# Performance work log

Measured on AMD Instinct MI355X. Metric: run time of the kernel, lower is better.

The kernel has to match this reference:

```python
import jax, jax.numpy as jnp
import numpy as np

DIM = 64
N_ITER = 2
NUM_USR = 50000
NUM_ENT = 200000
NUM_REL = 32
N_NEIGHBOR = 16
BATCH = 4096


def setup_inputs() -> dict:
    key = jax.random.key(0)
    ks = jax.random.split(key, 12)
    u = jax.random.randint(ks[0], (BATCH,), 0, NUM_USR)
    v = jax.random.randint(ks[1], (BATCH,), 0, NUM_ENT)
    adj = jax.random.randint(ks[2], (NUM_ENT, N_NEIGHBOR), 0, NUM_ENT)
    rel_adj = jax.random.randint(ks[3], (NUM_ENT, N_NEIGHBOR), 0, NUM_REL + 1)
    usr_emb = jax.random.normal(ks[4], (NUM_USR, DIM), dtype=jnp.float32)
    ent_emb = jax.random.normal(ks[5], (NUM_ENT, DIM), dtype=jnp.float32)
    rel_emb = jax.random.normal(ks[6], (NUM_REL + 1, DIM), dtype=jnp.float32)
    # per-hop aggregator Linear(dim, dim) weights (applied as x @ W + b)
    scale = 1.0 / np.sqrt(DIM)
    W0 = jax.random.uniform(ks[7], (DIM, DIM), jnp.float32, -scale, scale)
    b0 = jax.random.uniform(ks[8], (DIM,), jnp.float32, -scale, scale)
    W1 = jax.random.uniform(ks[9], (DIM, DIM), jnp.float32, -scale, scale)
    b1 = jax.random.uniform(ks[10], (DIM,), jnp.float32, -scale, scale)
    return {"u": u, "v": v, "adj": adj, "rel_adj": rel_adj,
            "usr_emb": usr_emb, "ent_emb": ent_emb, "rel_emb": rel_emb,
            "W0": W0, "b0": b0, "W1": W1, "b1": b1}


def reference(u, v, adj, rel_adj, usr_emb, ent_emb, rel_emb, W0, b0, W1, b1):
    B = u.shape[0]
    user = usr_emb[u]  # [B, D]

    # multi-hop neighbor index expansion
    entities = [v[:, None]]            # hop h: [B, n^h]
    relations = []
    for h in range(N_ITER):
        ne = adj[entities[h]].reshape(B, -1)      # [B, n^(h+1)]
        nr = rel_adj[entities[h]].reshape(B, -1)
        entities.append(ne)
        relations.append(nr)

    ent_vecs = [ent_emb[e] for e in entities]     # [B, n^h, D]
    rel_vecs = [rel_emb[r] for r in relations]

    Ws, bs = [W0, W1], [b0, b1]
    for i in range(N_ITER):
        act = jnp.tanh if i == N_ITER - 1 else jax.nn.sigmoid
        nxt = []
        for hop in range(N_ITER - i):
            sv = ent_vecs[hop]                                        # [B, m, D]
            nv = ent_vecs[hop + 1].reshape(B, -1, N_NEIGHBOR, DIM)    # [B, m, n, D]
            nr = rel_vecs[hop].reshape(B, -1, N_NEIGHBOR, DIM)        # [B, m, n, D]
            # user-relation attention over neighbors
            scores = jnp.einsum('bd,bmnd->bmn', user, nr)
            attn = jax.nn.softmax(scores, axis=-1)
            agg = jnp.einsum('bmn,bmnd->bmd', attn, nv)
            out = act((sv + agg) @ Ws[i] + bs[i])
            nxt.append(out)
        ent_vecs = nxt

    item = ent_vecs[0].reshape(B, DIM)
    return jax.nn.sigmoid(jnp.sum(user * item, axis=1))
```

## Files before the change

### kernel.cpp

```cpp
#include <hip/hip_runtime.h>

#define DIMN 64
#define NNB 16
#define NREL 33
#define WPB 4
#define XSTR 68

typedef float  floatx4 __attribute__((ext_vector_type(4)));
typedef short  shortx8 __attribute__((ext_vector_type(8)));

__device__ __forceinline__ float bcastf(float x, int lane) {
    return __int_as_float(__builtin_amdgcn_readlane(__float_as_int(x), lane));
}

__global__ void prep_w0_frags(const float* __restrict__ W0, unsigned short* __restrict__ wsp) {
    const int tid = blockIdx.x * blockDim.x + threadIdx.x;
    if (tid >= 512) return;
    const int l = tid & 63;
    const int t = (tid >> 6) & 3;
    const int ks = tid >> 8;
    const int k0 = ks * 32 + (l >> 4) * 8;
    const int n  = t * 16 + (l & 15);
    const unsigned base = ((unsigned)(ks * 4 + t) * 64 + l) * 8;
    #pragma unroll
    for (int j = 0; j < 8; ++j) {
        const float x = W0[(k0 + j) * DIMN + n];
        const unsigned u  = __float_as_uint(x);
        const unsigned uh = u & 0xFFFF0000u;
        const float lf = x - __uint_as_float(uh);
        wsp[base + j]        = (unsigned short)(u >> 16);
        wsp[4096 + base + j] = (unsigned short)(__float_as_uint(lf) >> 16);
    }
}

__global__ __launch_bounds__(64 * WPB, 4)
void kgs_kernel(const int* __restrict__ u, const int* __restrict__ v,
                const int* __restrict__ adj, const int* __restrict__ rel_adj,
                const float* __restrict__ usr_emb, const float* __restrict__ ent_emb,
                const float* __restrict__ rel_emb,
                const float* __restrict__ W0, const float* __restrict__ b0,
                const float* __restrict__ W1, const float* __restrict__ b1,
                const unsigned short* __restrict__ wsp,
                float* __restrict__ out, int B)
{
    const int tid = threadIdx.x;
    const int wid = tid >> 6;
    const int d   = tid & 63;
    int b = blockIdx.x * WPB + wid;
    if (b >= B) b = B - 1;
    const int n16 = d & 15;

    __shared__ __align__(16) float user_sh[WPB][DIMN];
    __shared__ float ur_sh[WPB][NREL + 7];
    __shared__ __align__(16) float xbuf[WPB][NNB * XSTR];

    const int uu = u[b];
    const int vv = v[b];

    const float user_d = usr_emb[uu * DIMN + d];
    const int e1n = adj[vv * NNB + n16];
    const int r1n = rel_adj[vv * NNB + n16];
    user_sh[wid][d] = user_d;

    if (d < NREL) {
        const float* re = rel_emb + d * DIMN;
        float acc = 0.f;
        #pragma unroll
        for (int k = 0; k < DIMN; k += 4) {
            const float4 uk = *(const float4*)(&user_sh[wid][k]);
            const float4 rk = *(const float4*)(re + k);
            acc = fmaf(uk.x, rk.x, acc);
            acc = fmaf(uk.y, rk.y, acc);
            acc = fmaf(uk.z, rk.z, acc);
            acc = fmaf(uk.w, rk.w, acc);
        }
        ur_sh[wid][d] = acc;
    }

    float sv_r[NNB];
    int   e2n_r[NNB], r2n_r[NNB];
    #pragma unroll
    for (int m = 0; m < NNB; ++m) {
        const int em = __builtin_amdgcn_readlane(e1n, m);
        sv_r[m]  = ent_emb[(size_t)em * DIMN + d];
        e2n_r[m] = adj[em * NNB + n16];
        r2n_r[m] = rel_adj[em * NNB + n16];
    }

    float attn[NNB];
    #pragma unroll
    for (int m = 0; m < NNB; ++m) {
        const float e = __expf(ur_sh[wid][r2n_r[m]]);
        float s = e;
        s += __shfl_xor(s, 1);
        s += __shfl_xor(s, 2);
        s += __shfl_xor(s, 4);
        s += __shfl_xor(s, 8);
        attn[m] = e * __builtin_amdgcn_rcpf(s);
    }

    float agg[NNB];
    #pragma unroll
    for (int m = 0; m < NNB; ++m) agg[m] = 0.f;
    #pragma unroll
    for (int m = 0; m < NNB; ++m) {
        #pragma unroll
        for (int n = 0; n < NNB; ++n) {
            const int en = __builtin_amdgcn_readlane(e2n_r[m], n);
            const float* rp = ent_emb + (size_t)en * DIMN;
            agg[m] = fmaf(bcastf(attn[m], n), rp[d], agg[m]);
        }
    }

    #pragma unroll
    for (int m = 0; m < NNB; ++m)
        xbuf[wid][m * XSTR + d] = sv_r[m] + agg[m];

    shortx8 Ahi[2], Alo[2];
    #pragma unroll
    for (int ks = 0; ks < 2; ++ks) {
        const float* ar = &xbuf[wid][(d & 15) * XSTR + ((d >> 4) * 8) + ks * 32];
        const floatx4 xa = *(const floatx4*)ar;
        const floatx4 xb = *(const floatx4*)(ar + 4);
        unsigned uh[8], ul[8];
        #pragma unroll
        for (int j = 0; j < 8; ++j) {
            const float x = (j < 4) ? xa[j] : xb[j - 4];
            const unsigned ub = __float_as_uint(x);
            uh[j] = ub & 0xFFFF0000u;
            ul[j] = __float_as_uint(x - __uint_as_float(uh[j]));
        }
        union { int i[4]; shortx8 s; } ch, cl;
        #pragma unroll
        for (int p = 0; p < 4; ++p) {
            ch.i[p] = (int)(uh[2 * p + 1] | (uh[2 * p] >> 16));
            cl.i[p] = (int)((ul[2 * p + 1] & 0xFFFF0000u) | (ul[2 * p] >> 16));
        }
        Ahi[ks] = ch.s;
        Alo[ks] = cl.s;
    }

    const shortx8* wf = (const shortx8*)wsp;
    floatx4 acc[4];
    #pragma unroll
    for (int t = 0; t < 4; ++t) acc[t] = (floatx4){0.f, 0.f, 0.f, 0.f};
    #pragma unroll
    for (int t = 0; t < 4; ++t) {
        #pragma unroll
        for (int ks = 0; ks < 2; ++ks) {
            const int f = ks * 4 + t;
            const shortx8 bhi = wf[f * 64 + d];
            const shortx8 blo = wf[512 + f * 64 + d];
            acc[t] = __builtin_amdgcn_mfma_f32_16x16x32_bf16(Ahi[ks], bhi, acc[t], 0, 0, 0);
            acc[t] = __builtin_amdgcn_mfma_f32_16x16x32_bf16(Ahi[ks], blo, acc[t], 0, 0, 0);
            acc[t] = __builtin_amdgcn_mfma_f32_16x16x32_bf16(Alo[ks], bhi, acc[t], 0, 0, 0);
        }
    }

    #pragma unroll
    for (int t = 0; t < 4; ++t) {
        const float bv = b0[t * 16 + (d & 15)];
        #pragma unroll
        for (int reg = 0; reg < 4; ++reg) {
            const float o = acc[t][reg] + bv;
            const float h = 1.f / (1.f + __expf(-o));
            const int m = (d >> 4) * 4 + reg;
            xbuf[wid][m * XSTR + t * 16 + (d & 15)] = h;
        }
    }
    float h1_r[NNB];
    #pragma unroll
    for (int n = 0; n < NNB; ++n)
        h1_r[n] = xbuf[wid][n * XSTR + d];

    const float sv0 = ent_emb[(size_t)vv * DIMN + d];
    const float e0 = __expf(ur_sh[wid][r1n]);
    float sum0 = e0;
    sum0 += __shfl_xor(sum0, 1);
    sum0 += __shfl_xor(sum0, 2);
    sum0 += __shfl_xor(sum0, 4);
    sum0 += __shfl_xor(sum0, 8);
    const float attn0 = e0 * __builtin_amdgcn_rcpf(sum0);

    float agg0 = 0.f, agg1 = 0.f;
    #pragma unroll
    for (int n = 0; n < NNB; ++n) {
        const float an = bcastf(attn0, n);
        agg0 = fmaf(an, sv_r[n], agg0);
        agg1 = fmaf(an, h1_r[n], agg1);
    }

    const float x0 = sv0 + agg0;
    float a0 = 0.f, a1 = 0.f, a2 = 0.f, a3 = 0.f;
    for (int k = 0; k < DIMN; k += 4) {
        const float* wr = W0 + k * DIMN;
        a0 = fmaf(bcastf(x0, k + 0), wr[d], a0);
        a1 = fmaf(bcastf(x0, k + 1), wr[DIMN + d], a1);
        a2 = fmaf(bcastf(x0, k + 2), wr[2 * DIMN + d], a2);
        a3 = fmaf(bcastf(x0, k + 3), wr[3 * DIMN + d], a3);
    }
    const float o0 = b0[d] + ((a0 + a1) + (a2 + a3));
    const float h0 = 1.f / (1.f + __expf(-o0));

    const float x1 = h0 + agg1;
    float c0 = 0.f, c1 = 0.f, c2 = 0.f, c3 = 0.f;
    for (int k = 0; k < DIMN; k += 4) {
        const float* wr = W1 + k * DIMN;
        c0 = fmaf(bcastf(x1, k + 0), wr[d], c0);
        c1 = fmaf(bcastf(x1, k + 1), wr[DIMN + d], c1);
        c2 = fmaf(bcastf(x1, k + 2), wr[2 * DIMN + d], c2);
        c3 = fmaf(bcastf(x1, k + 3), wr[3 * DIMN + d], c3);
    }
    const float o1 = b1[d] + ((c0 + c1) + (c2 + c3));
    const float item_d = 1.f - 2.f / (1.f + __expf(2.f * o1));

    float p = user_d * item_d;
    p += __shfl_xor(p, 1);
    p += __shfl_xor(p, 2);
    p += __shfl_xor(p, 4);
    p += __shfl_xor(p, 8);
    p += __shfl_xor(p, 16);
    p += __shfl_xor(p, 32);
    if (d == 0) out[b] = 1.f / (1.f + __expf(-p));
}

extern "C" void kernel_launch(void* const* d_in, const int* in_sizes, int n_in,
                              void* d_out, int out_size, void* d_ws, size_t ws_size,
                              hipStream_t stream) {
    const int*   u       = (const int*)d_in[0];
    const int*   v       = (const int*)d_in[1];
    const int*   adj     = (const int*)d_in[2];
    const int*   rel_adj = (const int*)d_in[3];
    const float* usr_emb = (const float*)d_in[4];
    const float* ent_emb = (const float*)d_in[5];
    const float* rel_emb = (const float*)d_in[6];
    const float* W0      = (const float*)d_in[7];
    const float* b0      = (const float*)d_in[8];
    const float* W1      = (const float*)d_in[9];
    const float* b1      = (const float*)d_in[10];
    float* out = (float*)d_out;
    unsigned short* wsp = (unsigned short*)d_ws;

    const int B = in_sizes[0];
    prep_w0_frags<<<dim3(2), dim3(256), 0, stream>>>(W0, wsp);
    const int grid = (B + WPB - 1) / WPB;
    kgs_kernel<<<dim3(grid), dim3(64 * WPB), 0, stream>>>(u, v, adj, rel_adj, usr_emb,
                                                          ent_emb, rel_emb, W0, b0, W1, b1,
                                                          wsp, out, B);
}
```

Before: 160.4 us.

## Split each batch row across two wavefronts to halve per-wave gather work

Each batch element is now handled by two wavefronts: each gathers and aggregates half of the 16 first-hop neighbors and computes half of the MFMA output tiles. The two halves exchange data through shared memory with block barriers, and one wave finishes the final hop. The goal is more memory-level parallelism and fewer registers per wave for the latency-bound gathers, at the cost of block-wide syncs and a wave that idles during the tail. Each wave also recomputes the user-relation scores redundantly.

```diff
diff --git a/kernel.cpp b/kernel.cpp
--- a/kernel.cpp
+++ b/kernel.cpp
@@ -3,7 +3,7 @@
 #define DIMN 64
 #define NNB 16
 #define NREL 33
-#define WPB 4
+#define MH 8
 #define XSTR 68
 
 typedef float  floatx4 __attribute__((ext_vector_type(4)));
@@ -33,7 +33,7 @@
     }
 }
 
-__global__ __launch_bounds__(64 * WPB, 4)
+__global__ __launch_bounds__(256, 8)
 void kgs_kernel(const int* __restrict__ u, const int* __restrict__ v,
                 const int* __restrict__ adj, const int* __restrict__ rel_adj,
                 const float* __restrict__ usr_emb, const float* __restrict__ ent_emb,
@@ -45,29 +45,32 @@
 {
     const int tid = threadIdx.x;
     const int wid = tid >> 6;
+    const int b_l = wid >> 1;
+    const int h   = wid & 1;
     const int d   = tid & 63;
-    int b = blockIdx.x * WPB + wid;
+    int b = blockIdx.x * 2 + b_l;
     if (b >= B) b = B - 1;
     const int n16 = d & 15;
 
-    __shared__ __align__(16) float user_sh[WPB][DIMN];
-    __shared__ float ur_sh[WPB][NREL + 7];
-    __shared__ __align__(16) float xbuf[WPB][NNB * XSTR];
+    __shared__ float ur_sh[4][NREL + 3];
+    __shared__ __align__(16) float sv_sh[2][NNB * XSTR];
+    __shared__ __align__(16) float xbuf[2][NNB * XSTR];
 
     const int uu = u[b];
     const int vv = v[b];
 
-    const float user_d = usr_emb[uu * DIMN + d];
+    const float user_d = usr_emb[(size_t)uu * DIMN + d];
     const int e1n = adj[vv * NNB + n16];
     const int r1n = rel_adj[vv * NNB + n16];
-    user_sh[wid][d] = user_d;
+    const float sv0 = ent_emb[(size_t)vv * DIMN + d];
 
     if (d < NREL) {
+        const float* up = usr_emb + (size_t)uu * DIMN;
         const float* re = rel_emb + d * DIMN;
         float acc = 0.f;
         #pragma unroll
         for (int k = 0; k < DIMN; k += 4) {
-            const float4 uk = *(const float4*)(&user_sh[wid][k]);
+            const float4 uk = *(const float4*)(up + k);
             const float4 rk = *(const float4*)(re + k);
             acc = fmaf(uk.x, rk.x, acc);
             acc = fmaf(uk.y, rk.y, acc);
@@ -77,49 +80,53 @@
         ur_sh[wid][d] = acc;
     }
 
-    float sv_r[NNB];
-    int   e2n_r[NNB], r2n_r[NNB];
-    #pragma unroll
-    for (int m = 0; m < NNB; ++m) {
+    float sv_r[MH];
+    int   e2n_r[MH], r2n_r[MH];
+    #pragma unroll
+    for (int mi = 0; mi < MH; ++mi) {
+        const int m  = h * MH + mi;
         const int em = __builtin_amdgcn_readlane(e1n, m);
-        sv_r[m]  = ent_emb[(size_t)em * DIMN + d];
-        e2n_r[m] = adj[em * NNB + n16];
-        r2n_r[m] = rel_adj[em * NNB + n16];
-    }
-
-    float attn[NNB];
-    #pragma unroll
-    for (int m = 0; m < NNB; ++m) {
-        const float e = __expf(ur_sh[wid][r2n_r[m]]);
+        sv_r[mi]  = ent_emb[(size_t)em * DIMN + d];
+        e2n_r[mi] = adj[em * NNB + n16];
+        r2n_r[mi] = rel_adj[em * NNB + n16];
+    }
+
+    float attn[MH];
+    #pragma unroll
+    for (int mi = 0; mi < MH; ++mi) {
+        const float e = __expf(ur_sh[wid][r2n_r[mi]]);
         float s = e;
         s += __shfl_xor(s, 1);
         s += __shfl_xor(s, 2);
         s += __shfl_xor(s, 4);
         s += __shfl_xor(s, 8);
-        attn[m] = e * __builtin_amdgcn_rcpf(s);
-    }
-
-    float agg[NNB];
-    #pragma unroll
-    for (int m = 0; m < NNB; ++m) agg[m] = 0.f;
-    #pragma unroll
-    for (int m = 0; m < NNB; ++m) {
+        attn[mi] = e * __builtin_amdgcn_rcpf(s);
+    }
+
+    float agg[MH];
+    #pragma unroll
+    for (int mi = 0; mi < MH; ++mi) agg[mi] = 0.f;
+    #pragma unroll
+    for (int mi = 0; mi < MH; ++mi) {
         #pragma unroll
         for (int n = 0; n < NNB; ++n) {
-            const int en = __builtin_amdgcn_readlane(e2n_r[m], n);
-            const float* rp = ent_emb + (size_t)en * DIMN;
-            agg[m] = fmaf(bcastf(attn[m], n), rp[d], agg[m]);
-        }
-    }
-
-    #pragma unroll
-    for (int m = 0; m < NNB; ++m)
-        xbuf[wid][m * XSTR + d] = sv_r[m] + agg[m];
+            const int en = __builtin_amdgcn_readlane(e2n_r[mi], n);
+            agg[mi] = fmaf(bcastf(attn[mi], n), ent_emb[(size_t)en * DIMN + d], agg[mi]);
+        }
+    }
+
+    #pragma unroll
+    for (int mi = 0; mi < MH; ++mi) {
+        const int m = h * MH + mi;
+        sv_sh[b_l][m * XSTR + d] = sv_r[mi];
+        xbuf[b_l][m * XSTR + d]  = sv_r[mi] + agg[mi];
+    }
+    __syncthreads();
 
     shortx8 Ahi[2], Alo[2];
     #pragma unroll
     for (int ks = 0; ks < 2; ++ks) {
-        const float* ar = &xbuf[wid][(d & 15) * XSTR + ((d >> 4) * 8) + ks * 32];
+        const float* ar = &xbuf[b_l][(d & 15) * XSTR + ((d >> 4) * 8) + ks * 32];
         const floatx4 xa = *(const floatx4*)ar;
         const floatx4 xb = *(const floatx4*)(ar + 4);
         unsigned uh[8], ul[8];
@@ -141,39 +148,39 @@
     }
 
     const shortx8* wf = (const shortx8*)wsp;
-    floatx4 acc[4];
-    #pragma unroll
-    for (int t = 0; t < 4; ++t) acc[t] = (floatx4){0.f, 0.f, 0.f, 0.f};
-    #pragma unroll
-    for (int t = 0; t < 4; ++t) {
+    floatx4 acc[2];
+    #pragma unroll
+    for (int tt = 0; tt < 2; ++tt) acc[tt] = (floatx4){0.f, 0.f, 0.f, 0.f};
+    #pragma unroll
+    for (int tt = 0; tt < 2; ++tt) {
+        const int t = 2 * h + tt;
         #pragma unroll
         for (int ks = 0; ks < 2; ++ks) {
             const int f = ks * 4 + t;
             const shortx8 bhi = wf[f * 64 + d];
             const shortx8 blo = wf[512 + f * 64 + d];
-            acc[t] = __builtin_amdgcn_mfma_f32_16x16x32_bf16(Ahi[ks], bhi, acc[t], 0, 0, 0);
-            acc[t] = __builtin_amdgcn_mfma_f32_16x16x32_bf16(Ahi[ks], blo, acc[t], 0, 0, 0);
-            acc[t] = __builtin_amdgcn_mfma_f32_16x16x32_bf16(Alo[ks], bhi, acc[t], 0, 0, 0);
-        }
-    }
-
-    #pragma unroll
-    for (int t = 0; t < 4; ++t) {
+            acc[tt] = __builtin_amdgcn_mfma_f32_16x16x32_bf16(Ahi[ks], bhi, acc[tt], 0, 0, 0);
+            acc[tt] = __builtin_amdgcn_mfma_f32_16x16x32_bf16(Ahi[ks], blo, acc[tt], 0, 0, 0);
+            acc[tt] = __builtin_amdgcn_mfma_f32_16x16x32_bf16(Alo[ks], bhi, acc[tt], 0, 0, 0);
+        }
+    }
+    __syncthreads();
+
+    #pragma unroll
+    for (int tt = 0; tt < 2; ++tt) {
+        const int t = 2 * h + tt;
         const float bv = b0[t * 16 + (d & 15)];
         #pragma unroll
         for (int reg = 0; reg < 4; ++reg) {
-            const float o = acc[t][reg] + bv;
-            const float h = 1.f / (1.f + __expf(-o));
+            const float o = acc[tt][reg] + bv;
             const int m = (d >> 4) * 4 + reg;
-            xbuf[wid][m * XSTR + t * 16 + (d & 15)] = h;
-        }
-    }
-    float h1_r[NNB];
-    #pragma unroll
-    for (int n = 0; n < NNB; ++n)
-        h1_r[n] = xbuf[wid][n * XSTR + d];
-
-    const float sv0 = ent_emb[(size_t)vv * DIMN + d];
+            xbuf[b_l][m * XSTR + t * 16 + (d & 15)] = 1.f / (1.f + __expf(-o));
+        }
+    }
+    __syncthreads();
+
+    if (h == 1) return;
+
     const float e0 = __expf(ur_sh[wid][r1n]);
     float sum0 = e0;
     sum0 += __shfl_xor(sum0, 1);
@@ -186,8 +193,8 @@
     #pragma unroll
     for (int n = 0; n < NNB; ++n) {
         const float an = bcastf(attn0, n);
-        agg0 = fmaf(an, sv_r[n], agg0);
-        agg1 = fmaf(an, h1_r[n], agg1);
+        agg0 = fmaf(an, sv_sh[b_l][n * XSTR + d], agg0);
+        agg1 = fmaf(an, xbuf[b_l][n * XSTR + d], agg1);
     }
 
     const float x0 = sv0 + agg0;
@@ -243,8 +250,8 @@
 
     const int B = in_sizes[0];
     prep_w0_frags<<<dim3(2), dim3(256), 0, stream>>>(W0, wsp);
-    const int grid = (B + WPB - 1) / WPB;
-    kgs_kernel<<<dim3(grid), dim3(64 * WPB), 0, stream>>>(u, v, adj, rel_adj, usr_emb,
-                                                          ent_emb, rel_emb, W0, b0, W1, b1,
-                                                          wsp, out, B);
-}
+    const int grid = (B + 1) / 2;
+    kgs_kernel<<<dim3(grid), dim3(256), 0, stream>>>(u, v, adj, rel_adj, usr_emb,
+                                                     ent_emb, rel_emb, W0, b0, W1, b1,
+                                                     wsp, out, B);
+}
```

After: 187.2 us. 16.7% more time.

## Vectorize neighbor embedding gathers with float4 loads and cross-quad shuffle reduction

Applied to the files above, without the earlier changes.

Rewrites the hop-2 neighbor gather so each 16-lane quad loads four distinct neighbor rows as float4, with attention weights fetched via shuffles and partial sums reduced across quads with xor shuffles. The first-hop entity rows are also loaded as float4 into a dedicated shared buffer instead of per-lane scalar loads into 16 registers. The aim is fewer, wider global load instructions and lower register pressure. In exchange it adds shuffle reductions, a second shared buffer and extra LDS reads in later stages.

```diff
diff --git a/kernel.cpp b/kernel.cpp
--- a/kernel.cpp
+++ b/kernel.cpp
@@ -43,24 +43,42 @@
                 const unsigned short* __restrict__ wsp,
                 float* __restrict__ out, int B)
 {
-    const int tid = threadIdx.x;
-    const int wid = tid >> 6;
-    const int d   = tid & 63;
+    const int tid  = threadIdx.x;
+    const int wid  = tid >> 6;
+    const int d    = tid & 63;
+    const int n16  = d & 15;
+    const int quad = d >> 4;
     int b = blockIdx.x * WPB + wid;
     if (b >= B) b = B - 1;
-    const int n16 = d & 15;
 
     __shared__ __align__(16) float user_sh[WPB][DIMN];
-    __shared__ float ur_sh[WPB][NREL + 7];
-    __shared__ __align__(16) float xbuf[WPB][NNB * XSTR];
+    __shared__ float ur_sh[WPB][NREL + 3];
+    __shared__ __align__(16) float sv_sh[WPB][NNB * XSTR];
+    __shared__ __align__(16) float gbuf[WPB][NNB * XSTR];
 
     const int uu = u[b];
     const int vv = v[b];
 
-    const float user_d = usr_emb[uu * DIMN + d];
+    const float user_d = usr_emb[(size_t)uu * DIMN + d];
     const int e1n = adj[vv * NNB + n16];
     const int r1n = rel_adj[vv * NNB + n16];
+    const float sv0 = ent_emb[(size_t)vv * DIMN + d];
     user_sh[wid][d] = user_d;
+
+    floatx4 svv[4];
+    #pragma unroll
+    for (int q = 0; q < 4; ++q) {
+        const int em = __shfl(e1n, 4 * q + quad);
+        svv[q] = *(const floatx4*)(ent_emb + (size_t)em * DIMN + 4 * n16);
+    }
+
+    int e2n_r[NNB], r2n_r[NNB];
+    #pragma unroll
+    for (int m = 0; m < NNB; ++m) {
+        const int em = __builtin_amdgcn_readlane(e1n, m);
+        e2n_r[m] = adj[em * NNB + n16];
+        r2n_r[m] = rel_adj[em * NNB + n16];
+    }
 
     if (d < NREL) {
         const float* re = rel_emb + d * DIMN;
@@ -77,15 +95,9 @@
         ur_sh[wid][d] = acc;
     }
 
-    float sv_r[NNB];
-    int   e2n_r[NNB], r2n_r[NNB];
-    #pragma unroll
-    for (int m = 0; m < NNB; ++m) {
-        const int em = __builtin_amdgcn_readlane(e1n, m);
-        sv_r[m]  = ent_emb[(size_t)em * DIMN + d];
-        e2n_r[m] = adj[em * NNB + n16];
-        r2n_r[m] = rel_adj[em * NNB + n16];
-    }
+    #pragma unroll
+    for (int q = 0; q < 4; ++q)
+        *(floatx4*)(&sv_sh[wid][(4 * q + quad) * XSTR + 4 * n16]) = svv[q];
 
     float attn[NNB];
     #pragma unroll
@@ -99,33 +111,41 @@
         attn[m] = e * __builtin_amdgcn_rcpf(s);
     }
 
-    float agg[NNB];
-    #pragma unroll
-    for (int m = 0; m < NNB; ++m) agg[m] = 0.f;
     #pragma unroll
     for (int m = 0; m < NNB; ++m) {
-        #pragma unroll
-        for (int n = 0; n < NNB; ++n) {
-            const int en = __builtin_amdgcn_readlane(e2n_r[m], n);
-            const float* rp = ent_emb + (size_t)en * DIMN;
-            agg[m] = fmaf(bcastf(attn[m], n), rp[d], agg[m]);
-        }
-    }
-
-    #pragma unroll
-    for (int m = 0; m < NNB; ++m)
-        xbuf[wid][m * XSTR + d] = sv_r[m] + agg[m];
+        floatx4 acc4 = (floatx4){0.f, 0.f, 0.f, 0.f};
+        #pragma unroll
+        for (int q = 0; q < 4; ++q) {
+            const int src = 4 * q + quad;
+            const int en  = __shfl(e2n_r[m], src);
+            const floatx4 g = *(const floatx4*)(ent_emb + (size_t)en * DIMN + 4 * n16);
+            const float aw = __shfl(attn[m], src);
+            acc4[0] = fmaf(aw, g[0], acc4[0]);
+            acc4[1] = fmaf(aw, g[1], acc4[1]);
+            acc4[2] = fmaf(aw, g[2], acc4[2]);
+            acc4[3] = fmaf(aw, g[3], acc4[3]);
+        }
+        #pragma unroll
+        for (int c = 0; c < 4; ++c) {
+            acc4[c] += __shfl_xor(acc4[c], 16);
+            acc4[c] += __shfl_xor(acc4[c], 32);
+        }
+        if (d < 16)
+            *(floatx4*)(&gbuf[wid][m * XSTR + 4 * d]) = acc4;
+    }
 
     shortx8 Ahi[2], Alo[2];
     #pragma unroll
     for (int ks = 0; ks < 2; ++ks) {
-        const float* ar = &xbuf[wid][(d & 15) * XSTR + ((d >> 4) * 8) + ks * 32];
-        const floatx4 xa = *(const floatx4*)ar;
-        const floatx4 xb = *(const floatx4*)(ar + 4);
+        const int off = (d & 15) * XSTR + quad * 8 + ks * 32;
+        const floatx4 sa = *(const floatx4*)(&sv_sh[wid][off]);
+        const floatx4 sb = *(const floatx4*)(&sv_sh[wid][off + 4]);
+        const floatx4 ga = *(const floatx4*)(&gbuf[wid][off]);
+        const floatx4 gb = *(const floatx4*)(&gbuf[wid][off + 4]);
         unsigned uh[8], ul[8];
         #pragma unroll
         for (int j = 0; j < 8; ++j) {
-            const float x = (j < 4) ? xa[j] : xb[j - 4];
+            const float x = (j < 4) ? (sa[j] + ga[j]) : (sb[j - 4] + gb[j - 4]);
             const unsigned ub = __float_as_uint(x);
             uh[j] = ub & 0xFFFF0000u;
             ul[j] = __float_as_uint(x - __uint_as_float(uh[j]));
@@ -159,21 +179,15 @@
 
     #pragma unroll
     for (int t = 0; t < 4; ++t) {
-        const float bv = b0[t * 16 + (d & 15)];
+        const float bv = b0[t * 16 + n16];
         #pragma unroll
         for (int reg = 0; reg < 4; ++reg) {
             const float o = acc[t][reg] + bv;
-            const float h = 1.f / (1.f + __expf(-o));
-            const int m = (d >> 4) * 4 + reg;
-            xbuf[wid][m * XSTR + t * 16 + (d & 15)] = h;
-        }
-    }
-    float h1_r[NNB];
-    #pragma unroll
-    for (int n = 0; n < NNB; ++n)
-        h1_r[n] = xbuf[wid][n * XSTR + d];
-
-    const float sv0 = ent_emb[(size_t)vv * DIMN + d];
+            const int m = quad * 4 + reg;
+            gbuf[wid][m * XSTR + t * 16 + n16] = 1.f / (1.f + __expf(-o));
+        }
+    }
+
     const float e0 = __expf(ur_sh[wid][r1n]);
     float sum0 = e0;
     sum0 += __shfl_xor(sum0, 1);
@@ -186,8 +200,8 @@
     #pragma unroll
     for (int n = 0; n < NNB; ++n) {
         const float an = bcastf(attn0, n);
-        agg0 = fmaf(an, sv_r[n], agg0);
-        agg1 = fmaf(an, h1_r[n], agg1);
+        agg0 = fmaf(an, sv_sh[wid][n * XSTR + d], agg0);
+        agg1 = fmaf(an, gbuf[wid][n * XSTR + d], agg1);
     }
 
     const float x0 = sv0 + agg0;
```

Measured after the change: 160.7 us. About the same (+0.2%).
